# Kernel tuning notes

Measured on AMD Instinct MI355X. Metric: run time of the kernel, lower is better.

## Reference

```python
import jax, jax.numpy as jnp
import numpy as np

D = 512        # latent_dim
CD = D // 2    # complex_dim = 256
R = 8          # low-rank
UD = 32        # u_dim
NY = 50        # n_y = 2*num_prod + num_inj
SEL_IN = D + UD + 1
H = 128
EPS = 1e-5


def _bn_relu(x, g, b):
    # BatchNorm1d (training mode: batch stats, biased var) + ReLU
    mu = jnp.mean(x, axis=0)
    var = jnp.mean((x - mu) ** 2, axis=0)
    return jax.nn.relu((x - mu) / jnp.sqrt(var + EPS) * g + b)


_LAYERS = [("0", SEL_IN, H), ("1", H, H), ("2", H, D),
           ("a", D, CD), ("o", D, CD),
           ("Ur", D, CD * R), ("Ui", D, CD * R),
           ("Vr", D, CD * R), ("Vi", D, CD * R),
           ("Br", D, CD * UD), ("Bi", D, CD * UD),
           ("Cr", D, NY * CD), ("Ci", D, NY * CD),
           ("D", D, NY * UD)]


def setup_inputs() -> dict:
    key = jax.random.key(0)
    B = 2048
    inp = {}
    k0, k1, k2, kp = jax.random.split(key, 4)
    inp["zt"] = jax.random.normal(k0, (B, D), jnp.float32)
    inp["dt"] = jax.random.uniform(k1, (B, 1), jnp.float32)
    inp["ut"] = jax.random.normal(k2, (B, UD), jnp.float32)
    ks = jax.random.split(kp, len(_LAYERS))
    for (name, fin, fout), k in zip(_LAYERS, ks):
        kw, kb = jax.random.split(k)
        inp["W" + name] = jax.random.normal(kw, (fin, fout), jnp.float32) * 0.02
        inp["b" + name] = jax.random.normal(kb, (fout,), jnp.float32) * 0.02
    # BN affine params for the two hidden selector layers
    inp["g0"] = jnp.ones((H,), jnp.float32)
    inp["be0"] = jnp.zeros((H,), jnp.float32)
    inp["g1"] = jnp.ones((H,), jnp.float32)
    inp["be1"] = jnp.zeros((H,), jnp.float32)
    return inp


def _fwd(zt, dt, ut, W0, b0, g0, be0, W1, b1, g1, be1, W2, b2,
         Wa, ba, Wo, bo, WUr, bUr, WUi, bUi, WVr, bVr, WVi, bVi,
         WBr, bBr, WBi, bBi, WCr, bCr, WCi, bCi, WD, bD):
    B = zt.shape[0]
    z = jax.lax.complex(zt[:, :CD], zt[:, CD:])               # [B, CD] complex
    x = jnp.concatenate([zt, ut, dt], axis=-1)                # [B, SEL_IN]
    h = _bn_relu(x @ W0 + b0, g0, be0)
    h = _bn_relu(h @ W1 + b1, g1, be1)
    hz = h @ W2 + b2                                          # [B, D]

    alpha = -jax.nn.softplus(hz @ Wa + ba)                    # [B, CD]
    omega = hz @ Wo + bo
    Lam = jnp.exp(jax.lax.complex(alpha, omega))              # |Lam| < 1

    U = jax.lax.complex(hz @ WUr + bUr, hz @ WUi + bUi).reshape(B, CD, R)
    V = jax.lax.complex(hz @ WVr + bVr, hz @ WVi + bVi).reshape(B, CD, R)
    # U (V^H z): [B, CD]
    t = jnp.einsum('bdr,bd->br', jnp.conj(V), z)
    low_rank = jnp.einsum('bdr,br->bd', U, t)

    Bt = jax.lax.complex(hz @ WBr + bBr, hz @ WBi + bBi).reshape(B, CD, UD)
    ut_dt = ut * dt                                           # [B, UD] real
    ut_dt_c = ut_dt.astype(Lam.dtype)
    z_next = Lam * z + low_rank + jnp.einsum('bdu,bu->bd', Bt, ut_dt_c)

    Ct = jax.lax.complex(hz @ WCr + bCr, hz @ WCi + bCi).reshape(B, NY, CD)
    Dt = (hz @ WD + bD).reshape(B, NY, UD)
    yt = jnp.einsum('bnd,bd->bn', Ct, z_next).real + jnp.einsum('bnu,bu->bn', Dt, ut_dt)

    z_next_real = jnp.concatenate([z_next.real, z_next.imag], axis=-1)  # [B, D]
    return z_next_real, yt


def reference(zt, dt, ut, W0, b0, g0, be0, W1, b1, g1, be1, W2, b2,
              Wa, ba, Wo, bo, WUr, bUr, WUi, bUi, WVr, bVr, WVi, bVi,
              WBr, bBr, WBi, bBi, WCr, bCr, WCi, bCi, WD, bD):
    return _fwd(zt, dt, ut, W0, b0, g0, be0, W1, b1, g1, be1, W2, b2,
                Wa, ba, Wo, bo, WUr, bUr, WUi, bUi, WVr, bVr, WVi, bVi,
                WBr, bBr, WBi, bBi, WCr, bCr, WCi, bCi, WD, bD)
```

## Files before the change

### kernel.cpp

```cpp
#include <hip/hip_runtime.h>
#include <hip/hip_bf16.h>
#include <cstdint>
#include <cstddef>


typedef __bf16 bf16;
typedef __bf16 bf16x8 __attribute__((ext_vector_type(8)));
typedef __bf16 bf16x4 __attribute__((ext_vector_type(4)));
typedef float f32x4 __attribute__((ext_vector_type(4)));

__device__ __forceinline__ void async16(const void* g, void* l) {
  __builtin_amdgcn_global_load_lds((const __attribute__((address_space(1))) void*)g,
                                   (__attribute__((address_space(3))) void*)l, 16, 0, 0);
}

__device__ __forceinline__ bool tile_map(int NT, int& m0, int& n0) {
  int L = blockIdx.x;
  int x = L & 7, s = L >> 3;
  int nt = ((s >> 4) << 3) + x;
  if (nt >= NT) return false;
  n0 = nt << 7;
  m0 = (s & 15) << 7;
  return true;
}

__device__ __forceinline__ void gemm_p3(const bf16* __restrict__ A,
                                        const bf16* __restrict__ Bw,
                                        int m0, int n0,
                                        bf16* lds, f32x4 acc[4][4]) {
  const int tid = threadIdx.x;
  const int w = tid >> 6, l = tid & 63;
  const int wm = (w >> 1) << 6, wn = (w & 1) << 6;
  const int fr = l & 15, q = l >> 4;

  const int c0 = tid, c1 = tid + 256;
  const int r0 = c0 >> 2, k0 = ((c0 & 3) ^ ((r0 >> 1) & 3)) << 3;
  const int r1 = c1 >> 2, k1 = ((c1 & 3) ^ ((r1 >> 1) & 3)) << 3;
  const bf16* a0 = A + (size_t)(m0 + r0) * 512 + k0;
  const bf16* a1 = A + (size_t)(m0 + r1) * 512 + k1;
  const bf16* b0 = Bw + (size_t)(n0 + r0) * 512 + k0;
  const bf16* b1 = Bw + (size_t)(n0 + r1) * 512 + k1;
  const int sw = (q ^ ((fr >> 1) & 3)) << 3;

#pragma unroll
  for (int mt = 0; mt < 4; ++mt)
#pragma unroll
    for (int nt = 0; nt < 4; ++nt) { f32x4 z = {0.f, 0.f, 0.f, 0.f}; acc[mt][nt] = z; }

  auto issue = [&](int kt, int p) {
    bf16* d = lds + p * 8192;
    async16(a0 + kt, d + (c0 << 3));
    async16(a1 + kt, d + (c1 << 3));
    async16(b0 + kt, d + 4096 + (c0 << 3));
    async16(b1 + kt, d + 4096 + (c1 << 3));
  };

  issue(0, 0);
  issue(32, 1);
#pragma unroll
  for (int it = 0; it < 16; ++it) {
    const int p = it % 3;
    if (it < 14) asm volatile("s_waitcnt vmcnt(4)" ::: "memory");
    else         asm volatile("s_waitcnt vmcnt(0)" ::: "memory");
    asm volatile("s_barrier" ::: "memory");
    if (it + 2 < 16) issue((it + 2) << 5, (it + 2) % 3);
    const bf16* ab = lds + p * 8192;
    const bf16* bb = ab + 4096;
    bf16x8 af[4], bfv[4];
#pragma unroll
    for (int mt = 0; mt < 4; ++mt)
      af[mt] = *(const bf16x8*)(ab + (wm + mt * 16 + fr) * 32 + sw);
#pragma unroll
    for (int nt = 0; nt < 4; ++nt)
      bfv[nt] = *(const bf16x8*)(bb + (wn + nt * 16 + fr) * 32 + sw);
#pragma unroll
    for (int mt = 0; mt < 4; ++mt)
#pragma unroll
      for (int nt = 0; nt < 4; ++nt)
        acc[mt][nt] = __builtin_amdgcn_mfma_f32_16x16x32_bf16(af[mt], bfv[nt],
                                                              acc[mt][nt], 0, 0, 0);
    asm volatile("s_waitcnt lgkmcnt(0)" ::: "memory");
  }
}

struct TEntry { const float* src; bf16* dst; int N, tile0, ntn; };
struct TArgs { TEntry e[11]; };

__global__ void k_transpose(TArgs a) {
  __shared__ float tile[64][65];
  int t = blockIdx.x;
  int ei = 0;
  while (ei < 10 && t >= a.e[ei + 1].tile0) ++ei;
  const TEntry E = a.e[ei];
  int lt = t - E.tile0;
  int tk = lt / E.ntn, tn = lt - tk * E.ntn;
  int k0 = tk << 6, n0 = tn << 6;
  int tid = threadIdx.x;
#pragma unroll
  for (int i = 0; i < 4; ++i) {
    int idx = tid + i * 256;
    int kk = idx >> 4, c4 = (idx & 15) << 2;
    const float4 v = *(const float4*)(E.src + (size_t)(k0 + kk) * E.N + n0 + c4);
    tile[c4 + 0][kk] = v.x; tile[c4 + 1][kk] = v.y;
    tile[c4 + 2][kk] = v.z; tile[c4 + 3][kk] = v.w;
  }
  __syncthreads();
#pragma unroll
  for (int i = 0; i < 4; ++i) {
    int idx = tid + i * 256;
    int nn = idx >> 4, k4 = (idx & 15) << 2;
    bf16x4 o;
    o[0] = (bf16)tile[nn][k4 + 0]; o[1] = (bf16)tile[nn][k4 + 1];
    o[2] = (bf16)tile[nn][k4 + 2]; o[3] = (bf16)tile[nn][k4 + 3];
    *(bf16x4*)(E.dst + (size_t)(n0 + nn) * 512 + k0 + k4) = o;
  }
}

__global__ void k_prep(const float* ba, const float* bo, const float* bVr, const float* bVi,
                       const float* bBr, const float* bBi, const float* bD,
                       const float* bUr, const float* bUi, const float* bCr, const float* bCi,
                       float* bbigA, float* bbigB, float* bbigC) {
  int i = blockIdx.x * 256 + threadIdx.x;
  if (i < 22656) {
    float v;
    if (i < 256) v = ba[i];
    else if (i < 512) v = bo[i - 256];
    else if (i < 2560) v = bVr[i - 512];
    else if (i < 4608) v = bVi[i - 2560];
    else if (i < 12800) v = bBr[i - 4608];
    else if (i < 20992) v = bBi[i - 12800];
    else if (i < 22592) v = bD[i - 20992];
    else v = 0.f;
    bbigA[i] = v;
  }
  int j = i - 22656;
  if (j >= 0 && j < 4096) bbigB[j] = (j < 2048) ? bUr[j] : bUi[j - 2048];
  int m = i - (22656 + 4096);
  if (m >= 0 && m < 25600) bbigC[m] = (m < 12800) ? bCr[m] : bCi[m - 12800];
}

__global__ void k_lin0(const float* __restrict__ zt, const float* __restrict__ dt,
                       const float* __restrict__ ut, const float* __restrict__ W0,
                       const float* __restrict__ b0, float* __restrict__ s0) {
  int i = blockIdx.x * 256 + threadIdx.x;
  int b = i >> 7, c = i & 127;
  const float* w = W0 + c;
  const float* x = zt + (size_t)b * 512;
  float a0 = b0[c], a1 = 0.f, a2 = 0.f, a3 = 0.f;
#pragma unroll 4
  for (int k = 0; k < 512; k += 4) {
    a0 = fmaf(x[k + 0], w[(size_t)(k + 0) * 128], a0);
    a1 = fmaf(x[k + 1], w[(size_t)(k + 1) * 128], a1);
    a2 = fmaf(x[k + 2], w[(size_t)(k + 2) * 128], a2);
    a3 = fmaf(x[k + 3], w[(size_t)(k + 3) * 128], a3);
  }
  const float* u = ut + (size_t)b * 32;
#pragma unroll
  for (int k = 0; k < 32; k += 4) {
    a0 = fmaf(u[k + 0], w[(size_t)(512 + k + 0) * 128], a0);
    a1 = fmaf(u[k + 1], w[(size_t)(512 + k + 1) * 128], a1);
    a2 = fmaf(u[k + 2], w[(size_t)(512 + k + 2) * 128], a2);
    a3 = fmaf(u[k + 3], w[(size_t)(512 + k + 3) * 128], a3);
  }
  a0 = fmaf(dt[b], w[(size_t)544 * 128], a0);
  s0[i] = (a0 + a1) + (a2 + a3);
}

__global__ void k_stats(const float* __restrict__ s, float* __restrict__ mu,
                        float* __restrict__ rstd) {
  int c = blockIdx.x;
  float sm = 0.f, sq = 0.f;
  for (int r = threadIdx.x; r < 2048; r += 256) {
    float v = s[(size_t)r * 128 + c];
    sm += v; sq += v * v;
  }
#pragma unroll
  for (int o = 32; o >= 1; o >>= 1) { sm += __shfl_down(sm, o); sq += __shfl_down(sq, o); }
  __shared__ float red[8];
  int w = threadIdx.x >> 6;
  if ((threadIdx.x & 63) == 0) { red[w] = sm; red[4 + w] = sq; }
  __syncthreads();
  if (threadIdx.x == 0) {
    float S = red[0] + red[1] + red[2] + red[3];
    float Q = red[4] + red[5] + red[6] + red[7];
    float m = S * (1.f / 2048.f);
    float var = Q * (1.f / 2048.f) - m * m;
    mu[c] = m;
    rstd[c] = rsqrtf(var + 1e-5f);
  }
}

__global__ void k_norm(float* __restrict__ s, const float* __restrict__ mu,
                       const float* __restrict__ rstd, const float* __restrict__ g,
                       const float* __restrict__ be) {
  int i = blockIdx.x * 256 + threadIdx.x;
  int c = i & 127;
  s[i] = fmaxf(fmaf((s[i] - mu[c]) * rstd[c], g[c], be[c]), 0.f);
}

__global__ void k_lin1(const float* __restrict__ h0, const float* __restrict__ W1,
                       const float* __restrict__ b1, float* __restrict__ s1) {
  int i = blockIdx.x * 256 + threadIdx.x;
  int b = i >> 7, c = i & 127;
  const float* w = W1 + c;
  const float* x = h0 + (size_t)b * 128;
  float a0 = b1[c], a1 = 0.f, a2 = 0.f, a3 = 0.f;
#pragma unroll 4
  for (int k = 0; k < 128; k += 4) {
    a0 = fmaf(x[k + 0], w[(size_t)(k + 0) * 128], a0);
    a1 = fmaf(x[k + 1], w[(size_t)(k + 1) * 128], a1);
    a2 = fmaf(x[k + 2], w[(size_t)(k + 2) * 128], a2);
    a3 = fmaf(x[k + 3], w[(size_t)(k + 3) * 128], a3);
  }
  s1[i] = (a0 + a1) + (a2 + a3);
}

__global__ void k_lin2(const float* __restrict__ h1, const float* __restrict__ W2,
                       const float* __restrict__ b2, bf16* __restrict__ hz) {
  int i = blockIdx.x * 256 + threadIdx.x;
  int b = i >> 9, c = i & 511;
  const float* w = W2 + c;
  const float* x = h1 + (size_t)b * 128;
  float a0 = b2[c], a1 = 0.f, a2 = 0.f, a3 = 0.f;
#pragma unroll 4
  for (int k = 0; k < 128; k += 4) {
    a0 = fmaf(x[k + 0], w[(size_t)(k + 0) * 512], a0);
    a1 = fmaf(x[k + 1], w[(size_t)(k + 1) * 512], a1);
    a2 = fmaf(x[k + 2], w[(size_t)(k + 2) * 512], a2);
    a3 = fmaf(x[k + 3], w[(size_t)(k + 3) * 512], a3);
  }
  hz[i] = (bf16)((a0 + a1) + (a2 + a3));
}

__global__ __launch_bounds__(256) void k_gemmA(
    const bf16* __restrict__ hz, const bf16* __restrict__ WT, const float* __restrict__ bias,
    const float* __restrict__ zt, const float* __restrict__ dt, const float* __restrict__ ut,
    float* __restrict__ pa, float* __restrict__ po,
    float* __restrict__ Bzr, float* __restrict__ Bzi,
    float* __restrict__ tbuf, float* __restrict__ ytout) {
  int m0, n0;
  if (!tile_map(177, m0, n0)) return;
  __shared__ __align__(16) bf16 lds[24576];
  f32x4 acc[4][4];
  gemm_p3(hz, WT, m0, n0, lds, acc);
  const int l = threadIdx.x & 63, w = threadIdx.x >> 6;
  const int wm = (w >> 1) << 6, wn = (w & 1) << 6;
  const int fr = l & 15, quad = l >> 4;
  const int ncol = n0 + wn;

  if (n0 < 512) {
    float* dst = (n0 < 256) ? pa : po;
    int cb = ncol - ((n0 < 256) ? 0 : 256);
#pragma unroll
    for (int mt = 0; mt < 4; ++mt)
#pragma unroll
      for (int j = 0; j < 4; ++j) {
        int b = m0 + wm + mt * 16 + quad * 4 + j;
#pragma unroll
        for (int nt = 0; nt < 4; ++nt) {
          int n = ncol + nt * 16 + fr;
          dst[(size_t)b * 256 + (cb + nt * 16 + fr)] = acc[mt][nt][j] + bias[n];
        }
      }
  } else if (n0 < 4608) {
    const bool isVr = n0 < 2560;
#pragma unroll
    for (int mt = 0; mt < 4; ++mt)
#pragma unroll
      for (int j = 0; j < 4; ++j) {
        int b = m0 + wm + mt * 16 + quad * 4 + j;
        float cre = 0.f, cim = 0.f;
#pragma unroll
        for (int nt = 0; nt < 4; ++nt) {
          int n = ncol + nt * 16 + fr;
          float v = acc[mt][nt][j] + bias[n];
          int d = ((n - 512) & 2047) >> 3;
          float zr = zt[(size_t)b * 512 + d], zi = zt[(size_t)b * 512 + 256 + d];
          if (isVr) { cre += v * zr; cim += v * zi; }
          else      { cre += v * zi; cim -= v * zr; }
        }
        cre += __shfl_xor(cre, 8);
        cim += __shfl_xor(cim, 8);
        if ((l & 8) == 0) {
          int r = fr & 7;
          atomicAdd(&tbuf[((size_t)b * 8 + r) * 2 + 0], cre);
          atomicAdd(&tbuf[((size_t)b * 8 + r) * 2 + 1], cim);
        }
      }
  } else if (n0 < 20992) {
    const bool isBr = n0 < 12800;
    float* dst = isBr ? Bzr : Bzi;
#pragma unroll
    for (int mt = 0; mt < 4; ++mt)
#pragma unroll
      for (int j = 0; j < 4; ++j) {
        int b = m0 + wm + mt * 16 + quad * 4 + j;
        float dtb = dt[b];
#pragma unroll
        for (int g = 0; g < 2; ++g) {
          float s = 0.f;
#pragma unroll
          for (int h = 0; h < 2; ++h) {
            int nt = g * 2 + h;
            int n = ncol + nt * 16 + fr;
            int base = (n - 4608) & 8191;
            float v = acc[mt][nt][j] + bias[n];
            s += v * ut[(size_t)b * 32 + (base & 31)];
          }
          s *= dtb;
          s += __shfl_xor(s, 1); s += __shfl_xor(s, 2);
          s += __shfl_xor(s, 4); s += __shfl_xor(s, 8);
          if ((l & 15) == 0) {
            int d = (((ncol + g * 32) - 4608) & 8191) >> 5;
            dst[(size_t)b * 256 + d] = s;
          }
        }
      }
  } else {
#pragma unroll
    for (int mt = 0; mt < 4; ++mt)
#pragma unroll
      for (int j = 0; j < 4; ++j) {
        int b = m0 + wm + mt * 16 + quad * 4 + j;
        float dtb = dt[b];
#pragma unroll
        for (int g = 0; g < 2; ++g) {
          float s = 0.f;
#pragma unroll
          for (int h = 0; h < 2; ++h) {
            int nt = g * 2 + h;
            int n = ncol + nt * 16 + fr;
            int base = n - 20992;
            float v = acc[mt][nt][j] + bias[n];
            s += v * ut[(size_t)b * 32 + (base & 31)];
          }
          s *= dtb;
          s += __shfl_xor(s, 1); s += __shfl_xor(s, 2);
          s += __shfl_xor(s, 4); s += __shfl_xor(s, 8);
          int nn = ((ncol + g * 32) - 20992) >> 5;
          if ((l & 15) == 0 && nn < 50) ytout[(size_t)b * 50 + nn] = s;
        }
      }
  }
}

__global__ __launch_bounds__(256) void k_gemmB(
    const bf16* __restrict__ hz, const bf16* __restrict__ WT, const float* __restrict__ bias,
    const float* __restrict__ tbuf, float* __restrict__ lr) {
  int m0, n0;
  if (!tile_map(32, m0, n0)) return;
  __shared__ __align__(16) bf16 lds[24576];
  f32x4 acc[4][4];
  gemm_p3(hz, WT, m0, n0, lds, acc);
  const int l = threadIdx.x & 63, w = threadIdx.x >> 6;
  const int wm = (w >> 1) << 6, wn = (w & 1) << 6;
  const int fr = l & 15, quad = l >> 4;
  const int ncol = n0 + wn;
  const bool isUr = n0 < 2048;
#pragma unroll
  for (int mt = 0; mt < 4; ++mt)
#pragma unroll
    for (int j = 0; j < 4; ++j) {
      int b = m0 + wm + mt * 16 + quad * 4 + j;
#pragma unroll
      for (int nt = 0; nt < 4; ++nt) {
        int n = ncol + nt * 16 + fr;
        int base = n & 2047;
        int r = base & 7, d = base >> 3;
        float v = acc[mt][nt][j] + bias[n];
        float tre = tbuf[((size_t)b * 8 + r) * 2], tim = tbuf[((size_t)b * 8 + r) * 2 + 1];
        float cre = isUr ? v * tre : -v * tim;
        float cim = isUr ? v * tim :  v * tre;
        cre += __shfl_xor(cre, 1); cre += __shfl_xor(cre, 2); cre += __shfl_xor(cre, 4);
        cim += __shfl_xor(cim, 1); cim += __shfl_xor(cim, 2); cim += __shfl_xor(cim, 4);
        if ((l & 7) == 0) {
          atomicAdd(&lr[((size_t)b * 256 + d) * 2 + 0], cre);
          atomicAdd(&lr[((size_t)b * 256 + d) * 2 + 1], cim);
        }
      }
    }
}

__global__ void k_assembleZ(const float* __restrict__ zt, const float* __restrict__ pa,
                            const float* __restrict__ po, const float* __restrict__ Bzr,
                            const float* __restrict__ Bzi, const float* __restrict__ lr,
                            float* __restrict__ zout, float* __restrict__ znr,
                            float* __restrict__ zni) {
  int i = blockIdx.x * 256 + threadIdx.x;
  int b = i >> 8, d = i & 255;
  float a = pa[i], o = po[i];
  float sp = fmaxf(a, 0.f) + log1pf(expf(-fabsf(a)));
  float mag = expf(-sp);
  float Lr = mag * cosf(o), Li = mag * sinf(o);
  float zr = zt[(size_t)b * 512 + d], zi = zt[(size_t)b * 512 + 256 + d];
  float re = fmaf(Lr, zr, -Li * zi) + Bzr[i] + lr[2 * i];
  float im = fmaf(Lr, zi,  Li * zr) + Bzi[i] + lr[2 * i + 1];
  zout[(size_t)b * 512 + d] = re;
  zout[(size_t)b * 512 + 256 + d] = im;
  znr[i] = re; zni[i] = im;
}

__global__ __launch_bounds__(256) void k_gemmC(
    const bf16* __restrict__ hz, const bf16* __restrict__ WT, const float* __restrict__ bias,
    const float* __restrict__ znr, const float* __restrict__ zni, float* __restrict__ ytout) {
  int m0, n0;
  if (!tile_map(200, m0, n0)) return;
  __shared__ __align__(16) bf16 lds[24576];
  f32x4 acc[4][4];
  gemm_p3(hz, WT, m0, n0, lds, acc);
  const int l = threadIdx.x & 63, w = threadIdx.x >> 6;
  const int wm = (w >> 1) << 6, wn = (w & 1) << 6;
  const int fr = l & 15, quad = l >> 4;
  const int ncol = n0 + wn;
  const bool isCr = n0 < 12800;
  const int nb = ncol - (isCr ? 0 : 12800);
  const int nn = nb >> 8;
#pragma unroll
  for (int mt = 0; mt < 4; ++mt)
#pragma unroll
    for (int j = 0; j < 4; ++j) {
      int b = m0 + wm + mt * 16 + quad * 4 + j;
      float s = 0.f;
#pragma unroll
      for (int nt = 0; nt < 4; ++nt) {
        int n = ncol + nt * 16 + fr;
        int d = (nb + nt * 16 + fr) & 255;
        float v = acc[mt][nt][j] + bias[n];
        s += isCr ? v * znr[(size_t)b * 256 + d] : -(v * zni[(size_t)b * 256 + d]);
      }
      s += __shfl_xor(s, 1); s += __shfl_xor(s, 2);
      s += __shfl_xor(s, 4); s += __shfl_xor(s, 8);
      if ((l & 15) == 0) atomicAdd(&ytout[(size_t)b * 50 + nn], s);
    }
}

extern "C" void kernel_launch(void* const* d_in, const int* in_sizes, int n_in,
                              void* d_out, int out_size, void* d_ws, size_t ws_size,
                              hipStream_t stream) {
  (void)in_sizes; (void)n_in; (void)out_size; (void)ws_size;
  const float* zt  = (const float*)d_in[0];
  const float* dt  = (const float*)d_in[1];
  const float* ut  = (const float*)d_in[2];
  const float* W0  = (const float*)d_in[3];  const float* b0  = (const float*)d_in[4];
  const float* W1  = (const float*)d_in[5];  const float* b1  = (const float*)d_in[6];
  const float* W2  = (const float*)d_in[7];  const float* b2  = (const float*)d_in[8];
  const float* Wa  = (const float*)d_in[9];  const float* ba  = (const float*)d_in[10];
  const float* Wo  = (const float*)d_in[11]; const float* bo  = (const float*)d_in[12];
  const float* WUr = (const float*)d_in[13]; const float* bUr = (const float*)d_in[14];
  const float* WUi = (const float*)d_in[15]; const float* bUi = (const float*)d_in[16];
  const float* WVr = (const float*)d_in[17]; const float* bVr = (const float*)d_in[18];
  const float* WVi = (const float*)d_in[19]; const float* bVi = (const float*)d_in[20];
  const float* WBr = (const float*)d_in[21]; const float* bBr = (const float*)d_in[22];
  const float* WBi = (const float*)d_in[23]; const float* bBi = (const float*)d_in[24];
  const float* WCr = (const float*)d_in[25]; const float* bCr = (const float*)d_in[26];
  const float* WCi = (const float*)d_in[27]; const float* bCi = (const float*)d_in[28];
  const float* WD  = (const float*)d_in[29]; const float* bD  = (const float*)d_in[30];
  const float* g0  = (const float*)d_in[31]; const float* be0 = (const float*)d_in[32];
  const float* g1  = (const float*)d_in[33]; const float* be1 = (const float*)d_in[34];

  char* ws = (char*)d_ws;
  bf16*  WTbig = (bf16*)(ws + 0);
  bf16*  WTU   = (bf16*)(ws + 23199744);
  bf16*  WTC   = (bf16*)(ws + 27394048);
  bf16*  hz    = (bf16*)(ws + 53608448);
  float* s0    = (float*)(ws + 55705600);
  float* s1    = (float*)(ws + 56754176);
  float* mu0   = (float*)(ws + 57802752);
  float* rstd0 = mu0 + 128;
  float* mu1   = mu0 + 256;
  float* rstd1 = mu0 + 384;
  float* bbigA = (float*)(ws + 57804800);
  float* bbigB = (float*)(ws + 57895424);
  float* bbigC = (float*)(ws + 57911808);
  float* pa    = (float*)(ws + 58014208);
  float* po    = (float*)(ws + 60111360);
  float* Bzr   = (float*)(ws + 62208512);
  float* Bzi   = (float*)(ws + 64305664);
  float* tbuf  = (float*)(ws + 66402816);
  float* lr    = (float*)(ws + 66533888);
  float* znr   = (float*)(ws + 70728192);
  float* zni   = (float*)(ws + 72825344);
  float* zout  = (float*)d_out;
  float* ytout = zout + 2048 * 512;

  k_prep<<<205, 256, 0, stream>>>(ba, bo, bVr, bVi, bBr, bBi, bD, bUr, bUi, bCr, bCi,
                                  bbigA, bbigB, bbigC);

  TArgs ta; int tile0 = 0; int idx = 0;
  auto add = [&](const float* src, bf16* dst, int N) {
    int ntn = N >> 6;
    ta.e[idx].src = src; ta.e[idx].dst = dst; ta.e[idx].N = N;
    ta.e[idx].tile0 = tile0; ta.e[idx].ntn = ntn;
    tile0 += ntn * 8; ++idx;
  };
  add(Wa,  WTbig + (size_t)0 * 512,     256);
  add(Wo,  WTbig + (size_t)256 * 512,   256);
  add(WVr, WTbig + (size_t)512 * 512,   2048);
  add(WVi, WTbig + (size_t)2560 * 512,  2048);
  add(WBr, WTbig + (size_t)4608 * 512,  8192);
  add(WBi, WTbig + (size_t)12800 * 512, 8192);
  add(WD,  WTbig + (size_t)20992 * 512, 1600);
  add(WUr, WTU,                         2048);
  add(WUi, WTU + (size_t)2048 * 512,    2048);
  add(WCr, WTC,                         12800);
  add(WCi, WTC + (size_t)12800 * 512,   12800);
  k_transpose<<<tile0, 256, 0, stream>>>(ta);

  hipMemsetAsync(tbuf, 0, 131072, stream);
  hipMemsetAsync(lr, 0, 4194304, stream);

  k_lin0<<<1024, 256, 0, stream>>>(zt, dt, ut, W0, b0, s0);
  k_stats<<<128, 256, 0, stream>>>(s0, mu0, rstd0);
  k_norm<<<1024, 256, 0, stream>>>(s0, mu0, rstd0, g0, be0);
  k_lin1<<<1024, 256, 0, stream>>>(s0, W1, b1, s1);
  k_stats<<<128, 256, 0, stream>>>(s1, mu1, rstd1);
  k_norm<<<1024, 256, 0, stream>>>(s1, mu1, rstd1, g1, be1);
  k_lin2<<<4096, 256, 0, stream>>>(s1, W2, b2, hz);

  k_gemmA<<<184 * 16, 256, 0, stream>>>(hz, WTbig, bbigA, zt, dt, ut,
                                        pa, po, Bzr, Bzi, tbuf, ytout);
  k_gemmB<<<32 * 16, 256, 0, stream>>>(hz, WTU, bbigB, tbuf, lr);
  k_assembleZ<<<2048, 256, 0, stream>>>(zt, pa, po, Bzr, Bzi, lr, zout, znr, zni);
  k_gemmC<<<200 * 16, 256, 0, stream>>>(hz, WTC, bbigC, znr, zni, ytout);
}
```

Measured before the change: 561.9 us.

## Use 256x256 tiles with 1024-thread blocks for the two large GEMMs

Adds a gemm256 routine that computes a 256x256 output tile per 16-wave block, with a triple-buffered async LDS pipeline. gemmA and gemmC switch to it, with a new tile mapping and the epilogue warp layout adjusted to 4x4 waves. The larger tiles cut how often hz and the weights are reloaded from global memory and reduce block count. The costs are fewer blocks for occupancy, a partial last column tile that is clamped for loads and bias-guarded, and 96KB of LDS per block.

```diff
diff --git a/kernel.cpp b/kernel.cpp
--- a/kernel.cpp
+++ b/kernel.cpp
@@ -14,7 +14,7 @@
                                    (__attribute__((address_space(3))) void*)l, 16, 0, 0);
 }
 
-__device__ __forceinline__ bool tile_map(int NT, int& m0, int& n0) {
+__device__ __forceinline__ bool tile_map16(int NT, int& m0, int& n0) {
   int L = blockIdx.x;
   int x = L & 7, s = L >> 3;
   int nt = ((s >> 4) << 3) + x;
@@ -22,6 +22,70 @@
   n0 = nt << 7;
   m0 = (s & 15) << 7;
   return true;
+}
+
+__device__ __forceinline__ bool tile_map8(int NT, int& m0, int& n0) {
+  int L = blockIdx.x;
+  int x = L & 7, s = L >> 3;
+  int nt = ((s >> 3) << 3) + x;
+  if (nt >= NT) return false;
+  n0 = nt << 8;
+  m0 = (s & 7) << 8;
+  return true;
+}
+
+__device__ __forceinline__ void gemm256(const bf16* __restrict__ A,
+                                        const bf16* __restrict__ Bw,
+                                        int m0, int n0, int nmax,
+                                        bf16* lds, f32x4 acc[4][4]) {
+  const int tid = threadIdx.x;
+  const int w = tid >> 6, l = tid & 63;
+  const int wm = (w >> 2) << 6, wn = (w & 3) << 6;
+  const int fr = l & 15, q = l >> 4;
+
+  const int r0 = tid >> 2, k0 = ((tid & 3) ^ ((r0 >> 1) & 3)) << 3;
+  int rb = n0 + r0; if (rb > nmax) rb = nmax;
+  const bf16* ag = A + (size_t)(m0 + r0) * 512 + k0;
+  const bf16* bg = Bw + (size_t)rb * 512 + k0;
+  const int sw = (q ^ ((fr >> 1) & 3)) << 3;
+
+#pragma unroll
+  for (int mt = 0; mt < 4; ++mt)
+#pragma unroll
+    for (int nt = 0; nt < 4; ++nt) { f32x4 z = {0.f, 0.f, 0.f, 0.f}; acc[mt][nt] = z; }
+
+  auto issue = [&](int kt, int p) {
+    bf16* d = lds + p * 16384;
+    async16(ag + kt, d + (tid << 3));
+    async16(bg + kt, d + 8192 + (tid << 3));
+  };
+
+  issue(0, 0);
+  issue(32, 1);
+#pragma unroll
+  for (int it = 0; it < 16; ++it) {
+    const int p = it % 3;
+    if (it < 14) asm volatile("s_waitcnt vmcnt(2)" ::: "memory");
+    else         asm volatile("s_waitcnt vmcnt(0)" ::: "memory");
+    asm volatile("s_barrier" ::: "memory");
+    if (it + 2 < 16) issue((it + 2) << 5, (it + 2) % 3);
+    const bf16* ab = lds + p * 16384;
+    const bf16* bb = ab + 8192;
+    bf16x8 af[4], bfv[4];
+#pragma unroll
+    for (int mt = 0; mt < 4; ++mt)
+      af[mt] = *(const bf16x8*)(ab + (wm + mt * 16 + fr) * 32 + sw);
+#pragma unroll
+    for (int nt = 0; nt < 4; ++nt)
+      bfv[nt] = *(const bf16x8*)(bb + (wn + nt * 16 + fr) * 32 + sw);
+#pragma unroll
+    for (int mt = 0; mt < 4; ++mt)
+#pragma unroll
+      for (int nt = 0; nt < 4; ++nt)
+        acc[mt][nt] = __builtin_amdgcn_mfma_f32_16x16x32_bf16(af[mt], bfv[nt],
+                                                              acc[mt][nt], 0, 0, 0);
+    asm volatile("s_waitcnt lgkmcnt(0)" ::: "memory");
+  }
 }
 
 __device__ __forceinline__ void gemm_p3(const bf16* __restrict__ A,
@@ -232,19 +296,19 @@
   hz[i] = (bf16)((a0 + a1) + (a2 + a3));
 }
 
-__global__ __launch_bounds__(256) void k_gemmA(
+__global__ __launch_bounds__(1024) void k_gemmA(
     const bf16* __restrict__ hz, const bf16* __restrict__ WT, const float* __restrict__ bias,
     const float* __restrict__ zt, const float* __restrict__ dt, const float* __restrict__ ut,
     float* __restrict__ pa, float* __restrict__ po,
     float* __restrict__ Bzr, float* __restrict__ Bzi,
     float* __restrict__ tbuf, float* __restrict__ ytout) {
   int m0, n0;
-  if (!tile_map(177, m0, n0)) return;
-  __shared__ __align__(16) bf16 lds[24576];
+  if (!tile_map8(89, m0, n0)) return;
+  __shared__ __align__(16) bf16 lds[49152];
   f32x4 acc[4][4];
-  gemm_p3(hz, WT, m0, n0, lds, acc);
+  gemm256(hz, WT, m0, n0, 22655, lds, acc);
   const int l = threadIdx.x & 63, w = threadIdx.x >> 6;
-  const int wm = (w >> 1) << 6, wn = (w & 1) << 6;
+  const int wm = (w >> 2) << 6, wn = (w & 3) << 6;
   const int fr = l & 15, quad = l >> 4;
   const int ncol = n0 + wn;
 
@@ -331,7 +395,8 @@
             int nt = g * 2 + h;
             int n = ncol + nt * 16 + fr;
             int base = n - 20992;
-            float v = acc[mt][nt][j] + bias[n];
+            float bv = (n < 22656) ? bias[n] : 0.f;
+            float v = acc[mt][nt][j] + bv;
             s += v * ut[(size_t)b * 32 + (base & 31)];
           }
           s *= dtb;
@@ -348,7 +413,7 @@
     const bf16* __restrict__ hz, const bf16* __restrict__ WT, const float* __restrict__ bias,
     const float* __restrict__ tbuf, float* __restrict__ lr) {
   int m0, n0;
-  if (!tile_map(32, m0, n0)) return;
+  if (!tile_map16(32, m0, n0)) return;
   __shared__ __align__(16) bf16 lds[24576];
   f32x4 acc[4][4];
   gemm_p3(hz, WT, m0, n0, lds, acc);
@@ -400,16 +465,16 @@
   znr[i] = re; zni[i] = im;
 }
 
-__global__ __launch_bounds__(256) void k_gemmC(
+__global__ __launch_bounds__(1024) void k_gemmC(
     const bf16* __restrict__ hz, const bf16* __restrict__ WT, const float* __restrict__ bias,
     const float* __restrict__ znr, const float* __restrict__ zni, float* __restrict__ ytout) {
   int m0, n0;
-  if (!tile_map(200, m0, n0)) return;
-  __shared__ __align__(16) bf16 lds[24576];
+  if (!tile_map8(100, m0, n0)) return;
+  __shared__ __align__(16) bf16 lds[49152];
   f32x4 acc[4][4];
-  gemm_p3(hz, WT, m0, n0, lds, acc);
+  gemm256(hz, WT, m0, n0, 25599, lds, acc);
   const int l = threadIdx.x & 63, w = threadIdx.x >> 6;
-  const int wm = (w >> 1) << 6, wn = (w & 1) << 6;
+  const int wm = (w >> 2) << 6, wn = (w & 3) << 6;
   const int fr = l & 15, quad = l >> 4;
   const int ncol = n0 + wn;
   const bool isCr = n0 < 12800;
@@ -517,9 +582,9 @@
   k_norm<<<1024, 256, 0, stream>>>(s1, mu1, rstd1, g1, be1);
   k_lin2<<<4096, 256, 0, stream>>>(s1, W2, b2, hz);
 
-  k_gemmA<<<184 * 16, 256, 0, stream>>>(hz, WTbig, bbigA, zt, dt, ut,
-                                        pa, po, Bzr, Bzi, tbuf, ytout);
+  k_gemmA<<<96 * 8, 1024, 0, stream>>>(hz, WTbig, bbigA, zt, dt, ut,
+                                       pa, po, Bzr, Bzi, tbuf, ytout);
   k_gemmB<<<32 * 16, 256, 0, stream>>>(hz, WTU, bbigB, tbuf, lr);
   k_assembleZ<<<2048, 256, 0, stream>>>(zt, pa, po, Bzr, Bzi, lr, zout, znr, zni);
-  k_gemmC<<<200 * 16, 256, 0, stream>>>(hz, WTC, bbigC, znr, zni, ytout);
-}
+  k_gemmC<<<104 * 8, 1024, 0, stream>>>(hz, WTC, bbigC, znr, zni, ytout);
+}
```

Measured after the change: 559.0 us. No clear change (-0.5%).

## Merge prep kernels into one launch, fuse BN into linears, double-buffer gemmC

Applied to the files above, without the earlier changes.

Merges the weight transpose, bias packing, buffer zeroing and first selector linear into a single multi-role kernel, replacing several launches and two memsets. Folds the BatchNorm+ReLU normalisation into the loads of the following linear layers, which removes the separate k_norm kernels. Switches gemmC to a two-stage LDS pipeline with a smaller shared buffer and a launch bound of 4 blocks per CU to raise occupancy. The trade-off is a shallower prefetch depth in gemmC and recomputing the normalisation in every thread that reads a row.

```diff
diff --git a/kernel.cpp b/kernel.cpp
--- a/kernel.cpp
+++ b/kernel.cpp
@@ -23,6 +23,7 @@
   m0 = (s & 15) << 7;
   return true;
 }
+
 
 __device__ __forceinline__ void gemm_p3(const bf16* __restrict__ A,
                                         const bf16* __restrict__ Bw,
@@ -83,87 +84,151 @@
   }
 }
 
+__device__ __forceinline__ void gemm_p2(const bf16* __restrict__ A,
+                                        const bf16* __restrict__ Bw,
+                                        int m0, int n0,
+                                        bf16* lds, f32x4 acc[4][4]) {
+  const int tid = threadIdx.x;
+  const int w = tid >> 6, l = tid & 63;
+  const int wm = (w >> 1) << 6, wn = (w & 1) << 6;
+  const int fr = l & 15, q = l >> 4;
+
+  const int c0 = tid, c1 = tid + 256;
+  const int r0 = c0 >> 2, k0 = ((c0 & 3) ^ ((r0 >> 1) & 3)) << 3;
+  const int r1 = c1 >> 2, k1 = ((c1 & 3) ^ ((r1 >> 1) & 3)) << 3;
+  const bf16* a0 = A + (size_t)(m0 + r0) * 512 + k0;
+  const bf16* a1 = A + (size_t)(m0 + r1) * 512 + k1;
+  const bf16* b0 = Bw + (size_t)(n0 + r0) * 512 + k0;
+  const bf16* b1 = Bw + (size_t)(n0 + r1) * 512 + k1;
+  const int sw = (q ^ ((fr >> 1) & 3)) << 3;
+
+#pragma unroll
+  for (int mt = 0; mt < 4; ++mt)
+#pragma unroll
+    for (int nt = 0; nt < 4; ++nt) { f32x4 z = {0.f, 0.f, 0.f, 0.f}; acc[mt][nt] = z; }
+
+  auto issue = [&](int kt, int p) {
+    bf16* d = lds + p * 8192;
+    async16(a0 + kt, d + (c0 << 3));
+    async16(a1 + kt, d + (c1 << 3));
+    async16(b0 + kt, d + 4096 + (c0 << 3));
+    async16(b1 + kt, d + 4096 + (c1 << 3));
+  };
+
+  issue(0, 0);
+#pragma unroll
+  for (int it = 0; it < 16; ++it) {
+    const int p = it & 1;
+    asm volatile("s_waitcnt vmcnt(0)" ::: "memory");
+    asm volatile("s_barrier" ::: "memory");
+    if (it + 1 < 16) issue((it + 1) << 5, p ^ 1);
+    const bf16* ab = lds + p * 8192;
+    const bf16* bb = ab + 4096;
+    bf16x8 af[4], bfv[4];
+#pragma unroll
+    for (int mt = 0; mt < 4; ++mt)
+      af[mt] = *(const bf16x8*)(ab + (wm + mt * 16 + fr) * 32 + sw);
+#pragma unroll
+    for (int nt = 0; nt < 4; ++nt)
+      bfv[nt] = *(const bf16x8*)(bb + (wn + nt * 16 + fr) * 32 + sw);
+#pragma unroll
+    for (int mt = 0; mt < 4; ++mt)
+#pragma unroll
+      for (int nt = 0; nt < 4; ++nt)
+        acc[mt][nt] = __builtin_amdgcn_mfma_f32_16x16x32_bf16(af[mt], bfv[nt],
+                                                              acc[mt][nt], 0, 0, 0);
+    asm volatile("s_waitcnt lgkmcnt(0)" ::: "memory");
+  }
+}
+
 struct TEntry { const float* src; bf16* dst; int N, tile0, ntn; };
-struct TArgs { TEntry e[11]; };
-
-__global__ void k_transpose(TArgs a) {
+struct P0Args {
+  TEntry e[11];
+  const float *ba, *bo, *bVr, *bVi, *bBr, *bBi, *bD, *bUr, *bUi, *bCr, *bCi;
+  float *bbigA, *bbigB, *bbigC;
+  float *tbuf, *lr;
+  const float *zt, *dt, *ut, *W0, *b0;
+  float* s0;
+};
+
+__global__ void k_p0(P0Args a) {
   __shared__ float tile[64][65];
-  int t = blockIdx.x;
-  int ei = 0;
-  while (ei < 10 && t >= a.e[ei + 1].tile0) ++ei;
-  const TEntry E = a.e[ei];
-  int lt = t - E.tile0;
-  int tk = lt / E.ntn, tn = lt - tk * E.ntn;
-  int k0 = tk << 6, n0 = tn << 6;
-  int tid = threadIdx.x;
-#pragma unroll
-  for (int i = 0; i < 4; ++i) {
-    int idx = tid + i * 256;
-    int kk = idx >> 4, c4 = (idx & 15) << 2;
-    const float4 v = *(const float4*)(E.src + (size_t)(k0 + kk) * E.N + n0 + c4);
-    tile[c4 + 0][kk] = v.x; tile[c4 + 1][kk] = v.y;
-    tile[c4 + 2][kk] = v.z; tile[c4 + 3][kk] = v.w;
-  }
-  __syncthreads();
-#pragma unroll
-  for (int i = 0; i < 4; ++i) {
-    int idx = tid + i * 256;
-    int nn = idx >> 4, k4 = (idx & 15) << 2;
-    bf16x4 o;
-    o[0] = (bf16)tile[nn][k4 + 0]; o[1] = (bf16)tile[nn][k4 + 1];
-    o[2] = (bf16)tile[nn][k4 + 2]; o[3] = (bf16)tile[nn][k4 + 3];
-    *(bf16x4*)(E.dst + (size_t)(n0 + nn) * 512 + k0 + k4) = o;
-  }
-}
-
-__global__ void k_prep(const float* ba, const float* bo, const float* bVr, const float* bVi,
-                       const float* bBr, const float* bBi, const float* bD,
-                       const float* bUr, const float* bUi, const float* bCr, const float* bCi,
-                       float* bbigA, float* bbigB, float* bbigC) {
-  int i = blockIdx.x * 256 + threadIdx.x;
-  if (i < 22656) {
-    float v;
-    if (i < 256) v = ba[i];
-    else if (i < 512) v = bo[i - 256];
-    else if (i < 2560) v = bVr[i - 512];
-    else if (i < 4608) v = bVi[i - 2560];
-    else if (i < 12800) v = bBr[i - 4608];
-    else if (i < 20992) v = bBi[i - 12800];
-    else if (i < 22592) v = bD[i - 20992];
-    else v = 0.f;
-    bbigA[i] = v;
-  }
-  int j = i - 22656;
-  if (j >= 0 && j < 4096) bbigB[j] = (j < 2048) ? bUr[j] : bUi[j - 2048];
-  int m = i - (22656 + 4096);
-  if (m >= 0 && m < 25600) bbigC[m] = (m < 12800) ? bCr[m] : bCi[m - 12800];
-}
-
-__global__ void k_lin0(const float* __restrict__ zt, const float* __restrict__ dt,
-                       const float* __restrict__ ut, const float* __restrict__ W0,
-                       const float* __restrict__ b0, float* __restrict__ s0) {
-  int i = blockIdx.x * 256 + threadIdx.x;
-  int b = i >> 7, c = i & 127;
-  const float* w = W0 + c;
-  const float* x = zt + (size_t)b * 512;
-  float a0 = b0[c], a1 = 0.f, a2 = 0.f, a3 = 0.f;
+  const int blk = blockIdx.x;
+  const int tid = threadIdx.x;
+
+  if (blk < 6536) {
+    int t = blk;
+    int ei = 0;
+    while (ei < 10 && t >= a.e[ei + 1].tile0) ++ei;
+    const TEntry E = a.e[ei];
+    int lt = t - E.tile0;
+    int tk = lt / E.ntn, tn = lt - tk * E.ntn;
+    int k0 = tk << 6, n0 = tn << 6;
+#pragma unroll
+    for (int i = 0; i < 4; ++i) {
+      int idx = tid + i * 256;
+      int kk = idx >> 4, c4 = (idx & 15) << 2;
+      const float4 v = *(const float4*)(E.src + (size_t)(k0 + kk) * E.N + n0 + c4);
+      tile[c4 + 0][kk] = v.x; tile[c4 + 1][kk] = v.y;
+      tile[c4 + 2][kk] = v.z; tile[c4 + 3][kk] = v.w;
+    }
+    __syncthreads();
+#pragma unroll
+    for (int i = 0; i < 4; ++i) {
+      int idx = tid + i * 256;
+      int nn = idx >> 4, k4 = (idx & 15) << 2;
+      bf16x4 o;
+      o[0] = (bf16)tile[nn][k4 + 0]; o[1] = (bf16)tile[nn][k4 + 1];
+      o[2] = (bf16)tile[nn][k4 + 2]; o[3] = (bf16)tile[nn][k4 + 3];
+      *(bf16x4*)(E.dst + (size_t)(n0 + nn) * 512 + k0 + k4) = o;
+    }
+  } else if (blk < 6741) {
+    int i = (blk - 6536) * 256 + tid;
+    if (i < 22656) {
+      float v;
+      if (i < 256) v = a.ba[i];
+      else if (i < 512) v = a.bo[i - 256];
+      else if (i < 2560) v = a.bVr[i - 512];
+      else if (i < 4608) v = a.bVi[i - 2560];
+      else if (i < 12800) v = a.bBr[i - 4608];
+      else if (i < 20992) v = a.bBi[i - 12800];
+      else if (i < 22592) v = a.bD[i - 20992];
+      else v = 0.f;
+      a.bbigA[i] = v;
+    }
+    int j = i - 22656;
+    if (j >= 0 && j < 4096) a.bbigB[j] = (j < 2048) ? a.bUr[j] : a.bUi[j - 2048];
+    int m = i - (22656 + 4096);
+    if (m >= 0 && m < 25600) a.bbigC[m] = (m < 12800) ? a.bCr[m] : a.bCi[m - 12800];
+  } else if (blk < 7797) {
+    int idx = (blk - 6741) * 256 + tid;
+    float4 z = {0.f, 0.f, 0.f, 0.f};
+    if (idx < 8192) *(float4*)(a.tbuf + idx * 4) = z;
+    else            *(float4*)(a.lr + (idx - 8192) * 4) = z;
+  } else {
+    int i = (blk - 7797) * 256 + tid;
+    int b = i >> 7, c = i & 127;
+    const float* w = a.W0 + c;
+    const float* x = a.zt + (size_t)b * 512;
+    float a0 = a.b0[c], a1 = 0.f, a2 = 0.f, a3 = 0.f;
 #pragma unroll 4
-  for (int k = 0; k < 512; k += 4) {
-    a0 = fmaf(x[k + 0], w[(size_t)(k + 0) * 128], a0);
-    a1 = fmaf(x[k + 1], w[(size_t)(k + 1) * 128], a1);
-    a2 = fmaf(x[k + 2], w[(size_t)(k + 2) * 128], a2);
-    a3 = fmaf(x[k + 3], w[(size_t)(k + 3) * 128], a3);
-  }
-  const float* u = ut + (size_t)b * 32;
-#pragma unroll
-  for (int k = 0; k < 32; k += 4) {
-    a0 = fmaf(u[k + 0], w[(size_t)(512 + k + 0) * 128], a0);
-    a1 = fmaf(u[k + 1], w[(size_t)(512 + k + 1) * 128], a1);
-    a2 = fmaf(u[k + 2], w[(size_t)(512 + k + 2) * 128], a2);
-    a3 = fmaf(u[k + 3], w[(size_t)(512 + k + 3) * 128], a3);
-  }
-  a0 = fmaf(dt[b], w[(size_t)544 * 128], a0);
-  s0[i] = (a0 + a1) + (a2 + a3);
+    for (int k = 0; k < 512; k += 4) {
+      a0 = fmaf(x[k + 0], w[(size_t)(k + 0) * 128], a0);
+      a1 = fmaf(x[k + 1], w[(size_t)(k + 1) * 128], a1);
+      a2 = fmaf(x[k + 2], w[(size_t)(k + 2) * 128], a2);
+      a3 = fmaf(x[k + 3], w[(size_t)(k + 3) * 128], a3);
+    }
+    const float* u = a.ut + (size_t)b * 32;
+#pragma unroll
+    for (int k = 0; k < 32; k += 4) {
+      a0 = fmaf(u[k + 0], w[(size_t)(512 + k + 0) * 128], a0);
+      a1 = fmaf(u[k + 1], w[(size_t)(512 + k + 1) * 128], a1);
+      a2 = fmaf(u[k + 2], w[(size_t)(512 + k + 2) * 128], a2);
+      a3 = fmaf(u[k + 3], w[(size_t)(512 + k + 3) * 128], a3);
+    }
+    a0 = fmaf(a.dt[b], w[(size_t)544 * 128], a0);
+    a.s0[i] = (a0 + a1) + (a2 + a3);
+  }
 }
 
 __global__ void k_stats(const float* __restrict__ s, float* __restrict__ mu,
@@ -190,44 +255,48 @@
   }
 }
 
-__global__ void k_norm(float* __restrict__ s, const float* __restrict__ mu,
+__global__ void k_lin1(const float* __restrict__ s0, const float* __restrict__ mu,
                        const float* __restrict__ rstd, const float* __restrict__ g,
-                       const float* __restrict__ be) {
-  int i = blockIdx.x * 256 + threadIdx.x;
-  int c = i & 127;
-  s[i] = fmaxf(fmaf((s[i] - mu[c]) * rstd[c], g[c], be[c]), 0.f);
-}
-
-__global__ void k_lin1(const float* __restrict__ h0, const float* __restrict__ W1,
+                       const float* __restrict__ be, const float* __restrict__ W1,
                        const float* __restrict__ b1, float* __restrict__ s1) {
   int i = blockIdx.x * 256 + threadIdx.x;
   int b = i >> 7, c = i & 127;
   const float* w = W1 + c;
-  const float* x = h0 + (size_t)b * 128;
+  const float* x = s0 + (size_t)b * 128;
   float a0 = b1[c], a1 = 0.f, a2 = 0.f, a3 = 0.f;
 #pragma unroll 4
   for (int k = 0; k < 128; k += 4) {
-    a0 = fmaf(x[k + 0], w[(size_t)(k + 0) * 128], a0);
-    a1 = fmaf(x[k + 1], w[(size_t)(k + 1) * 128], a1);
-    a2 = fmaf(x[k + 2], w[(size_t)(k + 2) * 128], a2);
-    a3 = fmaf(x[k + 3], w[(size_t)(k + 3) * 128], a3);
+    float h0 = fmaxf(fmaf((x[k + 0] - mu[k + 0]) * rstd[k + 0], g[k + 0], be[k + 0]), 0.f);
+    float h1 = fmaxf(fmaf((x[k + 1] - mu[k + 1]) * rstd[k + 1], g[k + 1], be[k + 1]), 0.f);
+    float h2 = fmaxf(fmaf((x[k + 2] - mu[k + 2]) * rstd[k + 2], g[k + 2], be[k + 2]), 0.f);
+    float h3 = fmaxf(fmaf((x[k + 3] - mu[k + 3]) * rstd[k + 3], g[k + 3], be[k + 3]), 0.f);
+    a0 = fmaf(h0, w[(size_t)(k + 0) * 128], a0);
+    a1 = fmaf(h1, w[(size_t)(k + 1) * 128], a1);
+    a2 = fmaf(h2, w[(size_t)(k + 2) * 128], a2);
+    a3 = fmaf(h3, w[(size_t)(k + 3) * 128], a3);
   }
   s1[i] = (a0 + a1) + (a2 + a3);
 }
 
-__global__ void k_lin2(const float* __restrict__ h1, const float* __restrict__ W2,
+__global__ void k_lin2(const float* __restrict__ s1, const float* __restrict__ mu,
+                       const float* __restrict__ rstd, const float* __restrict__ g,
+                       const float* __restrict__ be, const float* __restrict__ W2,
                        const float* __restrict__ b2, bf16* __restrict__ hz) {
   int i = blockIdx.x * 256 + threadIdx.x;
   int b = i >> 9, c = i & 511;
   const float* w = W2 + c;
-  const float* x = h1 + (size_t)b * 128;
+  const float* x = s1 + (size_t)b * 128;
   float a0 = b2[c], a1 = 0.f, a2 = 0.f, a3 = 0.f;
 #pragma unroll 4
   for (int k = 0; k < 128; k += 4) {
-    a0 = fmaf(x[k + 0], w[(size_t)(k + 0) * 512], a0);
-    a1 = fmaf(x[k + 1], w[(size_t)(k + 1) * 512], a1);
-    a2 = fmaf(x[k + 2], w[(size_t)(k + 2) * 512], a2);
-    a3 = fmaf(x[k + 3], w[(size_t)(k + 3) * 512], a3);
+    float h0 = fmaxf(fmaf((x[k + 0] - mu[k + 0]) * rstd[k + 0], g[k + 0], be[k + 0]), 0.f);
+    float h1 = fmaxf(fmaf((x[k + 1] - mu[k + 1]) * rstd[k + 1], g[k + 1], be[k + 1]), 0.f);
+    float h2 = fmaxf(fmaf((x[k + 2] - mu[k + 2]) * rstd[k + 2], g[k + 2], be[k + 2]), 0.f);
+    float h3 = fmaxf(fmaf((x[k + 3] - mu[k + 3]) * rstd[k + 3], g[k + 3], be[k + 3]), 0.f);
+    a0 = fmaf(h0, w[(size_t)(k + 0) * 512], a0);
+    a1 = fmaf(h1, w[(size_t)(k + 1) * 512], a1);
+    a2 = fmaf(h2, w[(size_t)(k + 2) * 512], a2);
+    a3 = fmaf(h3, w[(size_t)(k + 3) * 512], a3);
   }
   hz[i] = (bf16)((a0 + a1) + (a2 + a3));
 }
@@ -400,14 +469,14 @@
   znr[i] = re; zni[i] = im;
 }
 
-__global__ __launch_bounds__(256) void k_gemmC(
+__global__ __launch_bounds__(256, 4) void k_gemmC(
     const bf16* __restrict__ hz, const bf16* __restrict__ WT, const float* __restrict__ bias,
     const float* __restrict__ znr, const float* __restrict__ zni, float* __restrict__ ytout) {
   int m0, n0;
   if (!tile_map(200, m0, n0)) return;
-  __shared__ __align__(16) bf16 lds[24576];
+  __shared__ __align__(16) bf16 lds[16384];
   f32x4 acc[4][4];
-  gemm_p3(hz, WT, m0, n0, lds, acc);
+  gemm_p2(hz, WT, m0, n0, lds, acc);
   const int l = threadIdx.x & 63, w = threadIdx.x >> 6;
   const int wm = (w >> 1) << 6, wn = (w & 1) << 6;
   const int fr = l & 15, quad = l >> 4;
@@ -483,39 +552,40 @@
   float* zout  = (float*)d_out;
   float* ytout = zout + 2048 * 512;
 
-  k_prep<<<205, 256, 0, stream>>>(ba, bo, bVr, bVi, bBr, bBi, bD, bUr, bUi, bCr, bCi,
-                                  bbigA, bbigB, bbigC);
-
-  TArgs ta; int tile0 = 0; int idx = 0;
-  auto add = [&](const float* src, bf16* dst, int N) {
-    int ntn = N >> 6;
-    ta.e[idx].src = src; ta.e[idx].dst = dst; ta.e[idx].N = N;
-    ta.e[idx].tile0 = tile0; ta.e[idx].ntn = ntn;
-    tile0 += ntn * 8; ++idx;
-  };
-  add(Wa,  WTbig + (size_t)0 * 512,     256);
-  add(Wo,  WTbig + (size_t)256 * 512,   256);
-  add(WVr, WTbig + (size_t)512 * 512,   2048);
-  add(WVi, WTbig + (size_t)2560 * 512,  2048);
-  add(WBr, WTbig + (size_t)4608 * 512,  8192);
-  add(WBi, WTbig + (size_t)12800 * 512, 8192);
-  add(WD,  WTbig + (size_t)20992 * 512, 1600);
-  add(WUr, WTU,                         2048);
-  add(WUi, WTU + (size_t)2048 * 512,    2048);
-  add(WCr, WTC,                         12800);
-  add(WCi, WTC + (size_t)12800 * 512,   12800);
-  k_transpose<<<tile0, 256, 0, stream>>>(ta);
-
-  hipMemsetAsync(tbuf, 0, 131072, stream);
-  hipMemsetAsync(lr, 0, 4194304, stream);
-
-  k_lin0<<<1024, 256, 0, stream>>>(zt, dt, ut, W0, b0, s0);
+  P0Args pa0;
+  {
+    int tile0 = 0; int idx = 0;
+    auto add = [&](const float* src, bf16* dst, int N) {
+      int ntn = N >> 6;
+      pa0.e[idx].src = src; pa0.e[idx].dst = dst; pa0.e[idx].N = N;
+      pa0.e[idx].tile0 = tile0; pa0.e[idx].ntn = ntn;
+      tile0 += ntn * 8; ++idx;
+    };
+    add(Wa,  WTbig + (size_t)0 * 512,     256);
+    add(Wo,  WTbig + (size_t)256 * 512,   256);
+    add(WVr, WTbig + (size_t)512 * 512,   2048);
+    add(WVi, WTbig + (size_t)2560 * 512,  2048);
+    add(WBr, WTbig + (size_t)4608 * 512,  8192);
+    add(WBi, WTbig + (size_t)12800 * 512, 8192);
+    add(WD,  WTbig + (size_t)20992 * 512, 1600);
+    add(WUr, WTU,                         2048);
+    add(WUi, WTU + (size_t)2048 * 512,    2048);
+    add(WCr, WTC,                         12800);
+    add(WCi, WTC + (size_t)12800 * 512,   12800);
+  }
+  pa0.ba = ba; pa0.bo = bo; pa0.bVr = bVr; pa0.bVi = bVi; pa0.bBr = bBr;
+  pa0.bBi = bBi; pa0.bD = bD; pa0.bUr = bUr; pa0.bUi = bUi; pa0.bCr = bCr;
+  pa0.bCi = bCi;
+  pa0.bbigA = bbigA; pa0.bbigB = bbigB; pa0.bbigC = bbigC;
+  pa0.tbuf = tbuf; pa0.lr = lr;
+  pa0.zt = zt; pa0.dt = dt; pa0.ut = ut; pa0.W0 = W0; pa0.b0 = b0; pa0.s0 = s0;
+
+  k_p0<<<8821, 256, 0, stream>>>(pa0);
+
   k_stats<<<128, 256, 0, stream>>>(s0, mu0, rstd0);
-  k_norm<<<1024, 256, 0, stream>>>(s0, mu0, rstd0, g0, be0);
-  k_lin1<<<1024, 256, 0, stream>>>(s0, W1, b1, s1);
+  k_lin1<<<1024, 256, 0, stream>>>(s0, mu0, rstd0, g0, be0, W1, b1, s1);
   k_stats<<<128, 256, 0, stream>>>(s1, mu1, rstd1);
-  k_norm<<<1024, 256, 0, stream>>>(s1, mu1, rstd1, g1, be1);
-  k_lin2<<<4096, 256, 0, stream>>>(s1, W2, b2, hz);
+  k_lin2<<<4096, 256, 0, stream>>>(s1, mu1, rstd1, g1, be1, W2, b2, hz);
 
   k_gemmA<<<184 * 16, 256, 0, stream>>>(hz, WTbig, bbigA, zt, dt, ut,
                                         pa, po, Bzr, Bzi, tbuf, ytout);
```

Measured after the change: 561.1 us. Within noise of the previous version (-0.1%).
